# Performance work log

Measured on AMD Instinct MI355X. Metric: run time of the kernel, lower is better.

## Reference

```python
import jax, jax.numpy as jnp
import numpy as np

NUM_TERMS = 3
HIDDEN = 64
CLAMP_MIN = 1e-10


def _hermite_basis(x, num_terms):
    hs = [jnp.ones_like(x)]
    if num_terms > 1:
        hs.append(2.0 * x)
    for n in range(1, num_terms - 1):
        hs.append(2.0 * x * hs[n] - 2.0 * n * hs[n - 1])
    return jnp.stack(hs[:num_terms], axis=-1)  # (..., num_terms)


def setup_inputs() -> dict:
    key = jax.random.key(0)
    ks = jax.random.split(key, 7)
    B, S = 2048, 1024
    ys_coeffs = jax.random.normal(ks[0], (B, S, 2), dtype=jnp.float32)
    # scoring MLP params: Linear(3,64) -> ReLU -> Linear(64,64) -> ReLU -> Linear(64,num_terms)
    def lin(k, fan_in, fan_out):
        bound = 1.0 / np.sqrt(fan_in)
        kw, kb = jax.random.split(k)
        W = jax.random.uniform(kw, (fan_in, fan_out), minval=-bound, maxval=bound, dtype=jnp.float32)
        b = jax.random.uniform(kb, (fan_out,), minval=-bound, maxval=bound, dtype=jnp.float32)
        return W, b
    W1, b1 = lin(ks[1], 3, HIDDEN)
    W2, b2 = lin(ks[2], HIDDEN, HIDDEN)
    Wout, bout = lin(ks[3], HIDDEN, NUM_TERMS)
    return {"ys_coeffs": ys_coeffs, "W1": W1, "b1": b1, "W2": W2, "b2": b2,
            "Wout": Wout, "bout": bout}


def reference(ys_coeffs, W1, b1, W2, b2, Wout, bout):
    B, S, _ = ys_coeffs.shape
    timestamps = ys_coeffs[:, :, 0]
    values = ys_coeffs[:, :, 1]
    x0 = values[:, :-1]            # (B, S-1)
    xt = values[:, 1:]             # (B, S-1)
    t = timestamps[:, 1:]          # (B, S-1)
    feats = jnp.stack([xt, t, x0], axis=-1)           # (B, S-1, 3)
    h1 = jax.nn.relu(feats @ W1 + b1)                 # (B, S-1, 64)
    h2 = jax.nn.relu(h1 @ W2 + b2)                    # (B, S-1, 64)
    c_n = h2 @ Wout + bout                            # (B, S-1, num_terms)
    herm = _hermite_basis(xt, NUM_TERMS)              # (B, S-1, num_terms)
    p = jnp.sum(c_n * herm, axis=-1)                  # (B, S-1)
    p = jax.nn.softmax(p, axis=0)                     # softmax over batch dim (as in torch dim=0)
    log_likelihood = jnp.log(jnp.clip(p, CLAMP_MIN)).sum(axis=-1)  # (B,)
    return log_likelihood.mean()
```

## Files before the change

kernel.cpp:

```cpp
#include <hip/hip_runtime.h>
#include <hip/hip_bf16.h>

#define HIDDEN 64
#define BATCH 2048
#define SFULL 1024
#define SM1 1023
#define LN_CLAMP -23.025850929940457f
#define SP_PER 16

typedef __bf16 bf16x8 __attribute__((ext_vector_type(8)));
typedef float  f32x4  __attribute__((ext_vector_type(4)));
typedef float  f32x16 __attribute__((ext_vector_type(16)));
typedef short  s16x2  __attribute__((ext_vector_type(2)));

#define FRAG_UNITS 16

__device__ __forceinline__ int sig(int rg) {
    return 16 * ((rg >> 3) & 3) + 8 * ((rg >> 2) & 1) + (rg & 3) + 4 * (rg >> 5);
}

__device__ __forceinline__ unsigned pkt(float lo, float hi) {
    return __builtin_amdgcn_perm(__float_as_uint(hi), __float_as_uint(lo), 0x07060302u);
}
__device__ __forceinline__ unsigned rp(unsigned x) {
    s16x2 v = __builtin_bit_cast(s16x2, x);
    s16x2 z = {0, 0};
    v = __builtin_elementwise_max(v, z);
    return __builtin_bit_cast(unsigned, v);
}

__device__ __forceinline__ void relu_pack4(const f32x16 lo, const f32x16 hi, bf16x8* out) {
#pragma unroll
    for (int c = 0; c < 4; ++c) {
        union { unsigned u[4]; bf16x8 v; } r;
        r.u[0] = rp(pkt(lo[4 * c + 0], lo[4 * c + 1]));
        r.u[1] = rp(pkt(lo[4 * c + 2], lo[4 * c + 3]));
        r.u[2] = rp(pkt(hi[4 * c + 0], hi[4 * c + 1]));
        r.u[3] = rp(pkt(hi[4 * c + 2], hi[4 * c + 3]));
        out[c] = r.v;
    }
}

__device__ __forceinline__ bf16x8 featpk(float xt, float t, float x0) {
    union { unsigned u[4]; bf16x8 v; } r;
    r.u[0] = pkt(xt, t);
    r.u[1] = pkt(x0, 1.0f);
    r.u[2] = r.u[0]; r.u[3] = r.u[1];
    return r.v;
}

__global__ __launch_bounds__(256) void frag_setup_kernel(
    const float* __restrict__ W1, const float* __restrict__ b1,
    const float* __restrict__ W2, const float* __restrict__ b2,
    const float* __restrict__ Wout, char* __restrict__ F)
{
    const int l    = threadIdx.x & 63;
    const int wv   = threadIdx.x >> 6;
    const int pcol = l & 31;
    const int hi   = l >> 5;

    if (wv == 0) {
#pragma unroll
        for (int mt = 0; mt < 2; ++mt) {
            const int hout = sig(32 * mt + pcol);
            bf16x8 v;
#pragma unroll
            for (int j = 0; j < 8; ++j) {
                const int k = 8 * hi + j;
                v[j] = (k < 3) ? (__bf16)W1[k * 64 + hout]
                     : (k == 3) ? (__bf16)b1[hout] : (__bf16)0.0f;
            }
            *(bf16x8*)(F + ((mt * 64 + l) << 4)) = v;
        }
#pragma unroll
        for (int c = 0; c < 4; ++c) {
            bf16x8 v;
#pragma unroll
            for (int j = 0; j < 8; ++j) {
                const int k = 16 * c + 8 * hi + j;
                v[j] = (pcol < 3) ? (__bf16)Wout[k * 3 + pcol] : (__bf16)0.0f;
            }
            *(bf16x8*)(F + (((10 + c) * 64 + l) << 4)) = v;
        }
    } else if (wv == 1 || wv == 2) {
        const int mt = wv - 1;
        const int hout = sig(32 * mt + pcol);
#pragma unroll
        for (int c = 0; c < 4; ++c) {
            bf16x8 v;
#pragma unroll
            for (int j = 0; j < 8; ++j)
                v[j] = (__bf16)W2[(16 * c + 8 * hi + j) * 64 + hout];
            *(bf16x8*)(F + (((2 + mt * 4 + c) * 64 + l) << 4)) = v;
        }
    } else {
#pragma unroll
        for (int mt = 0; mt < 2; ++mt) {
            const int hout = sig(32 * mt + pcol);
            bf16x8 v;
#pragma unroll
            for (int j = 0; j < 8; ++j)
                v[j] = (hi == 0 && j == 0) ? (__bf16)b2[hout] : (__bf16)0.0f;
            *(bf16x8*)(F + (((14 + mt) * 64 + l) << 4)) = v;
        }
    }
}

__global__ __launch_bounds__(256, 3) void mlp_z_kernel(
    const float* __restrict__ ys,
    const char* __restrict__ F,
    const float* __restrict__ bout,
    float* __restrict__ z)
{
    const int l    = threadIdx.x & 63;
    const int wv   = threadIdx.x >> 6;
    const int pcol = l & 31;
    const int hi   = l >> 5;

    const int b   = (blockIdx.x * 4 + wv) * 32 + pcol;
    const int sp0 = blockIdx.y * SP_PER;
    const int omax = (SFULL - 1) - sp0;

    bf16x8 a1[2], a2[2][4], a3[4], a2b[2];
#pragma unroll
    for (int mt = 0; mt < 2; ++mt) {
        a1[mt]  = *(const bf16x8*)(F + ((mt * 64 + l) << 4));
        a2b[mt] = *(const bf16x8*)(F + (((14 + mt) * 64 + l) << 4));
#pragma unroll
        for (int c = 0; c < 4; ++c)
            a2[mt][c] = *(const bf16x8*)(F + (((2 + mt * 4 + c) * 64 + l) << 4));
    }
#pragma unroll
    for (int c = 0; c < 4; ++c)
        a3[c] = *(const bf16x8*)(F + (((10 + c) * 64 + l) << 4));

    bf16x8 Bone;
    {
        union { unsigned u[4]; bf16x8 v; } r;
        r.u[0] = (hi == 0) ? 0x3F80u : 0u;
        r.u[1] = 0u; r.u[2] = 0u; r.u[3] = 0u;
        Bone = r.v;
    }

    const float bo0 = bout[0], bo1 = bout[1], bo2 = bout[2];

    f32x16 zero16;
#pragma unroll
    for (int i = 0; i < 16; ++i) zero16[i] = 0.0f;

    const float2* base2 = reinterpret_cast<const float2*>(ys) + ((size_t)b * SFULL + sp0);
    float* zb = z + (size_t)sp0 * BATCH + b;

    float2 q0 = base2[0];
    float2 q1 = base2[min(1, omax)];
    float2 qn = base2[min(2, omax)];

    for (int it = 0; it < SP_PER; ++it) {
        const float2 qn2 = base2[min(it + 3, omax)];

        const float x0 = q0.y, t = q1.x, xt = q1.y;
        const bf16x8 f0 = featpk(xt, t, x0);

        f32x16 acc1_0 = __builtin_amdgcn_mfma_f32_32x32x16_bf16(a1[0], f0, zero16, 0, 0, 0);
        f32x16 acc1_1 = __builtin_amdgcn_mfma_f32_32x32x16_bf16(a1[1], f0, zero16, 0, 0, 0);

        f32x16 acc2_0 = __builtin_amdgcn_mfma_f32_32x32x16_bf16(a2b[0], Bone, zero16, 0, 0, 0);
        f32x16 acc2_1 = __builtin_amdgcn_mfma_f32_32x32x16_bf16(a2b[1], Bone, zero16, 0, 0, 0);

        bf16x8 h1f[4];
        relu_pack4(acc1_0, acc1_1, h1f);

#pragma unroll
        for (int c = 0; c < 4; ++c) {
            acc2_0 = __builtin_amdgcn_mfma_f32_32x32x16_bf16(a2[0][c], h1f[c], acc2_0, 0, 0, 0);
            acc2_1 = __builtin_amdgcn_mfma_f32_32x32x16_bf16(a2[1][c], h1f[c], acc2_1, 0, 0, 0);
        }

        bf16x8 h2f[4];
        relu_pack4(acc2_0, acc2_1, h2f);

        f32x16 acc3 = __builtin_amdgcn_mfma_f32_32x32x16_bf16(a3[0], h2f[0], zero16, 0, 0, 0);
#pragma unroll
        for (int c = 1; c < 4; ++c)
            acc3 = __builtin_amdgcn_mfma_f32_32x32x16_bf16(a3[c], h2f[c], acc3, 0, 0, 0);

        const float c0 = acc3[0] + bo0;
        const float c1 = acc3[1] + bo1;
        const float c2 = acc3[2] + bo2;
        const float zv = fmaf(c2, fmaf(4.0f * xt, xt, -2.0f), fmaf(c1, xt + xt, c0));

        if (l < 32 && sp0 + it < SM1)
            zb[(size_t)it * BATCH] = zv;

        q0 = q1; q1 = qn; qn = qn2;
    }
}

__device__ __forceinline__ float blk_reduce_max(float v) {
    __shared__ float s[4];
#pragma unroll
    for (int off = 32; off >= 1; off >>= 1) v = fmaxf(v, __shfl_xor(v, off));
    if ((threadIdx.x & 63) == 0) s[threadIdx.x >> 6] = v;
    __syncthreads();
    v = fmaxf(fmaxf(s[0], s[1]), fmaxf(s[2], s[3]));
    __syncthreads();
    return v;
}

__device__ __forceinline__ float blk_reduce_sum(float v) {
    __shared__ float s[4];
#pragma unroll
    for (int off = 32; off >= 1; off >>= 1) v += __shfl_xor(v, off);
    if ((threadIdx.x & 63) == 0) s[threadIdx.x >> 6] = v;
    __syncthreads();
    v = (s[0] + s[1]) + (s[2] + s[3]);
    __syncthreads();
    return v;
}

__global__ __launch_bounds__(256) void col_softmax_kernel(
    const float* __restrict__ z, float* __restrict__ colsum)
{
    const int sp = blockIdx.x;
    const int tid = threadIdx.x;
    const float* col = z + (size_t)sp * BATCH;

    float vals[8];
    float m = -3.4e38f;
#pragma unroll
    for (int i = 0; i < 8; ++i) {
        vals[i] = col[tid + 256 * i];
        m = fmaxf(m, vals[i]);
    }
    const float M = blk_reduce_max(m);

    float se = 0.0f;
#pragma unroll
    for (int i = 0; i < 8; ++i) se += __expf(vals[i] - M);
    const float S = blk_reduce_sum(se);
    const float L = __logf(S);

    float acc = 0.0f;
#pragma unroll
    for (int i = 0; i < 8; ++i) acc += fmaxf(vals[i] - M - L, LN_CLAMP);
    const float T = blk_reduce_sum(acc);
    if (tid == 0) colsum[sp] = T;
}

__global__ __launch_bounds__(256) void final_reduce_kernel(
    const float* __restrict__ colsum, float* __restrict__ out)
{
    const int tid = threadIdx.x;
    float v = 0.0f;
    for (int i = tid; i < SM1; i += 256) v += colsum[i];
    const float T = blk_reduce_sum(v);
    if (tid == 0) out[0] = T / (float)BATCH;
}

extern "C" void kernel_launch(void* const* d_in, const int* in_sizes, int n_in,
                              void* d_out, int out_size, void* d_ws, size_t ws_size,
                              hipStream_t stream) {
    const float* ys   = (const float*)d_in[0];
    const float* W1   = (const float*)d_in[1];
    const float* b1   = (const float*)d_in[2];
    const float* W2   = (const float*)d_in[3];
    const float* b2   = (const float*)d_in[4];
    const float* Wout = (const float*)d_in[5];
    const float* bout = (const float*)d_in[6];
    float* out = (float*)d_out;

    float* z      = (float*)d_ws;
    float* colsum = z + (size_t)SM1 * BATCH;
    size_t fo = ((size_t)SM1 * BATCH + SM1) * sizeof(float);
    fo = (fo + 15) & ~(size_t)15;
    char* F = (char*)d_ws + fo;

    frag_setup_kernel<<<1, 256, 0, stream>>>(W1, b1, W2, b2, Wout, F);
    dim3 grid1(16, 64);
    mlp_z_kernel<<<grid1, 256, 0, stream>>>(ys, F, bout, z);
    col_softmax_kernel<<<SM1, 256, 0, stream>>>(z, colsum);
    final_reduce_kernel<<<1, 256, 0, stream>>>(colsum, out);
}
```

Baseline: 42.83 us.

## Remap MLP lanes to sequence positions and store z batch-major

The MLP kernel now assigns the 32 MFMA columns to consecutive sequence positions of one batch row, and each wave walks 8 batch rows. This makes the ys loads contiguous instead of strided across batches. The intermediate z buffer is now stored as [batch][1024] so the writes are coalesced. The column softmax kernel therefore has to read z with a stride of 1024 floats, which trades coalesced loads there for coalesced loads and stores in the MLP kernel.

```diff
diff --git a/kernel.cpp b/kernel.cpp
--- a/kernel.cpp
+++ b/kernel.cpp
@@ -5,8 +5,8 @@
 #define BATCH 2048
 #define SFULL 1024
 #define SM1 1023
+#define ZSTR 1024
 #define LN_CLAMP -23.025850929940457f
-#define SP_PER 16
 
 typedef __bf16 bf16x8 __attribute__((ext_vector_type(8)));
 typedef float  f32x4  __attribute__((ext_vector_type(4)));
@@ -110,16 +110,17 @@
     const float* __restrict__ ys,
     const char* __restrict__ F,
     const float* __restrict__ bout,
-    float* __restrict__ z)
+    float* __restrict__ zp)
 {
     const int l    = threadIdx.x & 63;
     const int wv   = threadIdx.x >> 6;
     const int pcol = l & 31;
     const int hi   = l >> 5;
 
-    const int b   = (blockIdx.x * 4 + wv) * 32 + pcol;
-    const int sp0 = blockIdx.y * SP_PER;
-    const int omax = (SFULL - 1) - sp0;
+    const int b0   = blockIdx.x * 32 + wv * 8;
+    const int spt0 = blockIdx.y * 32;
+    const int sp   = spt0 + pcol;
+    const int o1   = min(pcol + 1, SM1 - spt0);
 
     bf16x8 a1[2], a2[2][4], a3[4], a2b[2];
 #pragma unroll
@@ -148,15 +149,18 @@
 #pragma unroll
     for (int i = 0; i < 16; ++i) zero16[i] = 0.0f;
 
-    const float2* base2 = reinterpret_cast<const float2*>(ys) + ((size_t)b * SFULL + sp0);
-    float* zb = z + (size_t)sp0 * BATCH + b;
-
-    float2 q0 = base2[0];
-    float2 q1 = base2[min(1, omax)];
-    float2 qn = base2[min(2, omax)];
-
-    for (int it = 0; it < SP_PER; ++it) {
-        const float2 qn2 = base2[min(it + 3, omax)];
+    const float2* rowp = reinterpret_cast<const float2*>(ys) + (size_t)b0 * SFULL + spt0;
+    float* zrow = zp + (size_t)b0 * ZSTR + spt0 + pcol;
+
+    float2 q0 = rowp[pcol];
+    float2 q1 = rowp[o1];
+
+    const bool do_store = (l < 32) && (sp < SM1);
+
+    for (int i = 0; i < 8; ++i) {
+        const float2* nrowp = rowp + SFULL;
+        float2 n0, n1;
+        if (i < 7) { n0 = nrowp[pcol]; n1 = nrowp[o1]; }
 
         const float x0 = q0.y, t = q1.x, xt = q1.y;
         const bf16x8 f0 = featpk(xt, t, x0);
@@ -164,11 +168,11 @@
         f32x16 acc1_0 = __builtin_amdgcn_mfma_f32_32x32x16_bf16(a1[0], f0, zero16, 0, 0, 0);
         f32x16 acc1_1 = __builtin_amdgcn_mfma_f32_32x32x16_bf16(a1[1], f0, zero16, 0, 0, 0);
 
+        bf16x8 h1f[4];
+        relu_pack4(acc1_0, acc1_1, h1f);
+
         f32x16 acc2_0 = __builtin_amdgcn_mfma_f32_32x32x16_bf16(a2b[0], Bone, zero16, 0, 0, 0);
         f32x16 acc2_1 = __builtin_amdgcn_mfma_f32_32x32x16_bf16(a2b[1], Bone, zero16, 0, 0, 0);
-
-        bf16x8 h1f[4];
-        relu_pack4(acc1_0, acc1_1, h1f);
 
 #pragma unroll
         for (int c = 0; c < 4; ++c) {
@@ -189,10 +193,10 @@
         const float c2 = acc3[2] + bo2;
         const float zv = fmaf(c2, fmaf(4.0f * xt, xt, -2.0f), fmaf(c1, xt + xt, c0));
 
-        if (l < 32 && sp0 + it < SM1)
-            zb[(size_t)it * BATCH] = zv;
-
-        q0 = q1; q1 = qn; qn = qn2;
+        if (do_store) zrow[0] = zv;
+        zrow += ZSTR;
+        rowp = nrowp;
+        if (i < 7) { q0 = n0; q1 = n1; }
     }
 }
 
@@ -219,17 +223,17 @@
 }
 
 __global__ __launch_bounds__(256) void col_softmax_kernel(
-    const float* __restrict__ z, float* __restrict__ colsum)
+    const float* __restrict__ zp, float* __restrict__ colsum)
 {
     const int sp = blockIdx.x;
     const int tid = threadIdx.x;
-    const float* col = z + (size_t)sp * BATCH;
+    const float* col = zp + sp;
 
     float vals[8];
     float m = -3.4e38f;
 #pragma unroll
     for (int i = 0; i < 8; ++i) {
-        vals[i] = col[tid + 256 * i];
+        vals[i] = col[(size_t)(tid + 256 * i) * ZSTR];
         m = fmaxf(m, vals[i]);
     }
     const float M = blk_reduce_max(m);
@@ -269,15 +273,15 @@
     const float* bout = (const float*)d_in[6];
     float* out = (float*)d_out;
 
-    float* z      = (float*)d_ws;
-    float* colsum = z + (size_t)SM1 * BATCH;
-    size_t fo = ((size_t)SM1 * BATCH + SM1) * sizeof(float);
+    float* zp     = (float*)d_ws;
+    float* colsum = zp + (size_t)BATCH * ZSTR;
+    size_t fo = ((size_t)BATCH * ZSTR + SM1) * sizeof(float);
     fo = (fo + 15) & ~(size_t)15;
     char* F = (char*)d_ws + fo;
 
     frag_setup_kernel<<<1, 256, 0, stream>>>(W1, b1, W2, b2, Wout, F);
-    dim3 grid1(16, 64);
-    mlp_z_kernel<<<grid1, 256, 0, stream>>>(ys, F, bout, z);
-    col_softmax_kernel<<<SM1, 256, 0, stream>>>(z, colsum);
+    dim3 grid1(64, 32);
+    mlp_z_kernel<<<grid1, 256, 0, stream>>>(ys, F, bout, zp);
+    col_softmax_kernel<<<SM1, 256, 0, stream>>>(zp, colsum);
     final_reduce_kernel<<<1, 256, 0, stream>>>(colsum, out);
 }
```

Result: slower. 60.28 us (+40.8%).
